# Kernel optimization log

Hardware: AMD Instinct MI355X
Metric: run time of the kernel (lower is better)

## Reference

```python
import jax, jax.numpy as jnp
import numpy as np
import math

B, S, DIN, DQ, DV = 8, 2048, 1024, 1024, 1024


def setup_inputs() -> dict:
    key = jax.random.key(0)
    ks = jax.random.split(key, 9)
    c_q = math.sqrt(6.0 / (DIN + DQ))
    c_v = math.sqrt(6.0 / (DIN + DV))
    query = jax.random.normal(ks[0], (B, S, DIN), dtype=jnp.float32)
    key_t = jax.random.normal(ks[1], (B, S, DIN), dtype=jnp.float32)
    value = jax.random.normal(ks[2], (B, S, DIN), dtype=jnp.float32)
    # Linear weights stored as [in, out] for x @ W; uniform init per module
    Wq = jax.random.uniform(ks[3], (DIN, DQ), jnp.float32, -c_q, c_q)
    Wk = jax.random.uniform(ks[4], (DIN, DQ), jnp.float32, -c_q, c_q)
    Wv = jax.random.uniform(ks[5], (DIN, DV), jnp.float32, -c_v, c_v)
    bq = jax.random.uniform(ks[6], (DQ,), jnp.float32, -c_q, c_q)
    bk = jax.random.uniform(ks[7], (DQ,), jnp.float32, -c_q, c_q)
    bv = jax.random.uniform(ks[8], (DV,), jnp.float32, -c_v, c_v)
    # causal mask: True where attention is disallowed (masked_fill semantics)
    mask = jnp.broadcast_to(jnp.triu(jnp.ones((S, S), dtype=bool), k=1), (B, S, S))
    return {"query": query, "key": key_t, "value": value,
            "Wq": Wq, "bq": bq, "Wk": Wk, "bk": bk, "Wv": Wv, "bv": bv,
            "mask": mask}


def reference(query, key, value, Wq, bq, Wk, bk, Wv, bv, mask):
    q = query @ Wq + bq                       # [B,S,DQ]
    k = key @ Wk + bk                         # [B,S,DQ]
    v = value @ Wv + bv                       # [B,S,DV]
    scores = jnp.einsum('bsd,btd->bst', q, k) / math.sqrt(DQ)  # [B,S,S]
    scores = jnp.where(mask, jnp.float32(-1e9), scores)
    weights = jax.nn.softmax(scores, axis=2)
    y = jnp.einsum('bst,btd->bsd', weights, v)  # [B,S,DV]
    return y
```

## Files before the change

kernel.cpp:

```cpp
#include <hip/hip_runtime.h>


typedef unsigned short u16;
typedef unsigned int   u32;
typedef float f32x4 __attribute__((ext_vector_type(4)));
typedef short s16x8 __attribute__((ext_vector_type(8)));

__device__ __forceinline__ u16 f2bf(float x) {
  u32 u = __builtin_bit_cast(u32, x);
  u += 0x7fffu + ((u >> 16) & 1u);
  return (u16)(u >> 16);
}

__device__ __forceinline__ void gld_lds16(const u16* g, u16* l) {
  __builtin_amdgcn_global_load_lds((const __attribute__((address_space(1))) void*)g,
                                   (__attribute__((address_space(3))) void*)l,
                                   16, 0, 0);
}

__global__ __launch_bounds__(256) void cvt_bf16_3(const float* __restrict__ i0,
                                                  const float* __restrict__ i1,
                                                  const float* __restrict__ i2,
                                                  u16* __restrict__ out, long X) {
  const float* in = blockIdx.y == 0 ? i0 : (blockIdx.y == 1 ? i1 : i2);
  long i = (long)blockIdx.x * 256 + threadIdx.x;
  float4 v = ((const float4*)in)[i];
  ushort4 o;
  o.x = f2bf(v.x); o.y = f2bf(v.y); o.z = f2bf(v.z); o.w = f2bf(v.w);
  ((ushort4*)(out + blockIdx.y * X))[i] = o;
}

__global__ __launch_bounds__(256) void transpose_w3(const float* __restrict__ w0,
                                                    const float* __restrict__ w1,
                                                    const float* __restrict__ w2,
                                                    u16* __restrict__ Wt,
                                                    int K, int N, long WN) {
  __shared__ u16 t[32][33];
  const float* W = blockIdx.z == 0 ? w0 : (blockIdx.z == 1 ? w1 : w2);
  u16* out = Wt + blockIdx.z * WN;
  int n0 = blockIdx.x * 32, k0 = blockIdx.y * 32;
  int tx = threadIdx.x & 31, ty = threadIdx.x >> 5;
  for (int r = ty; r < 32; r += 8)
    t[r][tx] = f2bf(W[(long)(k0 + r) * N + n0 + tx]);
  __syncthreads();
  for (int r = ty; r < 32; r += 8)
    out[(long)(n0 + r) * K + k0 + tx] = t[tx][r];
}

__global__ __launch_bounds__(256) void transpose_v(const u16* __restrict__ v,
                                                   u16* __restrict__ vt,
                                                   int S, int D) {
  __shared__ u16 t[32][33];
  long b = blockIdx.z;
  const u16* vb = v + b * S * D;
  u16* vtb = vt + b * S * D;
  int d0 = blockIdx.x * 32, s0 = blockIdx.y * 32;
  int tx = threadIdx.x & 31, ty = threadIdx.x >> 5;
  for (int r = ty; r < 32; r += 8)
    t[r][tx] = vb[(long)(s0 + r) * D + d0 + tx];
  __syncthreads();
  for (int r = ty; r < 32; r += 8)
    vtb[(long)(d0 + r) * S + s0 + tx] = t[tx][r];
}

__device__ __forceinline__ void gemm_core(const u16* __restrict__ At,
                                          const u16* __restrict__ Bt,
                                          int lda, int ldb, int ktEnd,
                                          f32x4 (&acc)[4][4],
                                          u16* lA, u16* lB) {
  const int tid = threadIdx.x;
  const int lane = tid & 63, half = lane >> 4, l16 = lane & 15;
  const int wave = tid >> 6;
  const int wm = (wave >> 1) * 64, wn = (wave & 1) * 64;

  const int c0 = tid, c1 = tid + 256;
  const int r0 = c0 >> 2, kp0 = (c0 & 3) ^ ((c0 >> 3) & 3);
  const int r1 = c1 >> 2, kp1 = (c1 & 3) ^ ((c1 >> 3) & 3);
  const u16* gA0 = At + (long)r0 * lda + kp0 * 8;
  const u16* gA1 = At + (long)r1 * lda + kp1 * 8;
  const u16* gB0 = Bt + (long)r0 * ldb + kp0 * 8;
  const u16* gB1 = Bt + (long)r1 * ldb + kp1 * 8;
  u16* lA0 = lA + c0 * 8; u16* lA1 = lA + c1 * 8;
  u16* lB0 = lB + c0 * 8; u16* lB1 = lB + c1 * 8;
  const int swz = (half ^ ((l16 >> 1) & 3)) * 8;

  for (int kt = 0; kt < ktEnd; ++kt) {
    const int k0 = kt * 32;
    gld_lds16(gA0 + k0, lA0);
    gld_lds16(gA1 + k0, lA1);
    gld_lds16(gB0 + k0, lB0);
    gld_lds16(gB1 + k0, lB1);
    __syncthreads();
    s16x8 af[4], bfr[4];
#pragma unroll
    for (int mi = 0; mi < 4; ++mi)
      af[mi] = *(const s16x8*)&lA[(wm + mi * 16 + l16) * 32 + swz];
#pragma unroll
    for (int ni = 0; ni < 4; ++ni)
      bfr[ni] = *(const s16x8*)&lB[(wn + ni * 16 + l16) * 32 + swz];
#pragma unroll
    for (int mi = 0; mi < 4; ++mi)
#pragma unroll
      for (int ni = 0; ni < 4; ++ni)
        acc[mi][ni] = __builtin_amdgcn_mfma_f32_16x16x32_bf16(af[mi], bfr[ni], acc[mi][ni], 0, 0, 0);
    __syncthreads();
  }
}

struct ProjPtrs {
  const u16* A[3];
  const u16* B[3];
  u16* C[3];
  const float* bias[3];
};

__global__ __launch_bounds__(256, 2)
void gemm_proj(ProjPtrs p, int lda, int ldb, int ldc, int kTiles) {
  const int bn = blockIdx.x, bm = blockIdx.y, bz = blockIdx.z;
  __shared__ u16 lA[128 * 32], lB[128 * 32];
  f32x4 acc[4][4];
#pragma unroll
  for (int i = 0; i < 4; ++i)
#pragma unroll
    for (int j = 0; j < 4; ++j) { f32x4 z = {0.f, 0.f, 0.f, 0.f}; acc[i][j] = z; }

  gemm_core(p.A[bz] + (long)bm * 128 * lda, p.B[bz] + (long)bn * 128 * ldb,
            lda, ldb, kTiles, acc, lA, lB);

  const int lane = threadIdx.x & 63, half = lane >> 4, l16 = lane & 15;
  const int wave = threadIdx.x >> 6;
  const int wm = (wave >> 1) * 64, wn = (wave & 1) * 64;
  const int colBase = bn * 128 + wn + l16;
  const int rowBase = bm * 128 + wm + half * 4;
  u16* Cb = p.C[bz];
  const float* bias = p.bias[bz];
#pragma unroll
  for (int mi = 0; mi < 4; ++mi)
#pragma unroll
    for (int ni = 0; ni < 4; ++ni) {
      int col = colBase + ni * 16;
      float bv = bias[col];
#pragma unroll
      for (int r = 0; r < 4; ++r)
        Cb[(long)(rowBase + mi * 16 + r) * ldc + col] = f2bf(acc[mi][ni][r] + bv);
    }
}

__global__ __launch_bounds__(256, 2)
void gemm_scores(const u16* __restrict__ q, const u16* __restrict__ k,
                 float* __restrict__ scores, int ld, long sQK, long sSC,
                 int kTiles, float scale) {
  const int t = blockIdx.x, bz = blockIdx.y;
  int bm = (int)((sqrtf(8.f * t + 1.f) - 1.f) * 0.5f);
  while ((bm + 1) * (bm + 2) / 2 <= t) ++bm;
  while (bm * (bm + 1) / 2 > t) --bm;
  const int bn = t - bm * (bm + 1) / 2;

  __shared__ u16 lA[128 * 32], lB[128 * 32];
  f32x4 acc[4][4];
#pragma unroll
  for (int i = 0; i < 4; ++i)
#pragma unroll
    for (int j = 0; j < 4; ++j) { f32x4 z = {0.f, 0.f, 0.f, 0.f}; acc[i][j] = z; }

  gemm_core(q + (long)bz * sQK + (long)bm * 128 * ld,
            k + (long)bz * sQK + (long)bn * 128 * ld,
            ld, ld, kTiles, acc, lA, lB);

  const int lane = threadIdx.x & 63, half = lane >> 4, l16 = lane & 15;
  const int wave = threadIdx.x >> 6;
  const int wm = (wave >> 1) * 64, wn = (wave & 1) * 64;
  float* Cb = scores + (long)bz * sSC;
  const int colBase = bn * 128 + wn + l16;
  const int rowBase = bm * 128 + wm + half * 4;
#pragma unroll
  for (int mi = 0; mi < 4; ++mi)
#pragma unroll
    for (int ni = 0; ni < 4; ++ni) {
      int col = colBase + ni * 16;
#pragma unroll
      for (int r = 0; r < 4; ++r)
        Cb[(long)(rowBase + mi * 16 + r) * 2048 + col] = acc[mi][ni][r] * scale;
    }
}

__global__ __launch_bounds__(256, 2)
void gemm_pv(const u16* __restrict__ P, const u16* __restrict__ vT,
             float* __restrict__ y, int lda, int ldb, int ldc,
             long sP, long sV, long sY, int kTiles) {
  const int bn = blockIdx.x, bz = blockIdx.z;
  const int bm = gridDim.y - 1 - blockIdx.y;
  int ktEnd = (bm + 1) * 4; if (ktEnd > kTiles) ktEnd = kTiles;

  __shared__ u16 lA[128 * 32], lB[128 * 32];
  f32x4 acc[4][4];
#pragma unroll
  for (int i = 0; i < 4; ++i)
#pragma unroll
    for (int j = 0; j < 4; ++j) { f32x4 z = {0.f, 0.f, 0.f, 0.f}; acc[i][j] = z; }

  gemm_core(P + (long)bz * sP + (long)bm * 128 * lda,
            vT + (long)bz * sV + (long)bn * 128 * ldb,
            lda, ldb, ktEnd, acc, lA, lB);

  const int lane = threadIdx.x & 63, half = lane >> 4, l16 = lane & 15;
  const int wave = threadIdx.x >> 6;
  const int wm = (wave >> 1) * 64, wn = (wave & 1) * 64;
  float* Cb = y + (long)bz * sY;
  const int colBase = bn * 128 + wn + l16;
  const int rowBase = bm * 128 + wm + half * 4;
#pragma unroll
  for (int mi = 0; mi < 4; ++mi)
#pragma unroll
    for (int ni = 0; ni < 4; ++ni) {
      int col = colBase + ni * 16;
#pragma unroll
      for (int r = 0; r < 4; ++r)
        Cb[(long)(rowBase + mi * 16 + r) * ldc + col] = acc[mi][ni][r];
    }
}

__global__ __launch_bounds__(256) void softmax_causal(const float* __restrict__ scores,
                                                      u16* __restrict__ P, int S) {
  __shared__ float buf[2048];
  __shared__ float red[4];
  const int tid = threadIdx.x;
  const long row = blockIdx.x;
  const int i = (int)(row & (S - 1));
  const int n = i + 1;
  const float* srow = scores + row * S;
  u16* prow = P + row * S;

  float m = -1e30f;
  for (int j = tid; j < n; j += 256) { float x = srow[j]; buf[j] = x; m = fmaxf(m, x); }
  for (int o = 32; o > 0; o >>= 1) m = fmaxf(m, __shfl_down(m, o));
  if ((tid & 63) == 0) red[tid >> 6] = m;
  __syncthreads();
  m = fmaxf(fmaxf(red[0], red[1]), fmaxf(red[2], red[3]));
  __syncthreads();
  float s = 0.f;
  for (int j = tid; j < n; j += 256) { float e = __expf(buf[j] - m); buf[j] = e; s += e; }
  for (int o = 32; o > 0; o >>= 1) s += __shfl_down(s, o);
  if ((tid & 63) == 0) red[tid >> 6] = s;
  __syncthreads();
  s = red[0] + red[1] + red[2] + red[3];
  float inv = 1.f / s;
  for (int j = tid; j < n; j += 256) prow[j] = f2bf(buf[j] * inv);
  const int zend = ((i >> 7) + 1) << 7;
  for (int j = n + tid; j < zend; j += 256) prow[j] = 0;
}

extern "C" void kernel_launch(void* const* d_in, const int* in_sizes, int n_in,
                              void* d_out, int out_size, void* d_ws, size_t ws_size,
                              hipStream_t stream) {
  const int B = 8, S = 2048, DIN = 1024, DQ = 1024, DV = 1024;
  const long X  = (long)B * S * DIN;
  const long WN = (long)DIN * DQ;

  const float* query = (const float*)d_in[0];
  const float* key   = (const float*)d_in[1];
  const float* value = (const float*)d_in[2];
  const float* Wq = (const float*)d_in[3];
  const float* bq = (const float*)d_in[4];
  const float* Wk = (const float*)d_in[5];
  const float* bk = (const float*)d_in[6];
  const float* Wv = (const float*)d_in[7];
  const float* bv = (const float*)d_in[8];

  u16* w = (u16*)d_ws;
  u16* xq = w;
  u16* WT = w + 3 * X;
  const long R1 = 3 * X + 3 * WN;
  u16* vbuf = w + R1;
  u16* q  = w + R1 + X;
  u16* k  = w + R1 + 2 * X;
  u16* vT = w + R1 + 3 * X;
  float* scores = (float*)d_ws;
  u16* P = q;

  dim3 blk(256);
  cvt_bf16_3<<<dim3(X / 1024, 3), blk, 0, stream>>>(query, key, value, xq, X);
  transpose_w3<<<dim3(DQ / 32, DIN / 32, 3), blk, 0, stream>>>(Wq, Wk, Wv, WT, DIN, DQ, WN);

  ProjPtrs pp;
  pp.A[0] = xq; pp.A[1] = xq + X; pp.A[2] = xq + 2 * X;
  pp.B[0] = WT; pp.B[1] = WT + WN; pp.B[2] = WT + 2 * WN;
  pp.C[0] = q;  pp.C[1] = k;      pp.C[2] = vbuf;
  pp.bias[0] = bq; pp.bias[1] = bk; pp.bias[2] = bv;
  gemm_proj<<<dim3(DQ / 128, (B * S) / 128, 3), blk, 0, stream>>>(
      pp, DIN, DIN, DQ, DIN / 32);

  transpose_v<<<dim3(DV / 32, S / 32, B), blk, 0, stream>>>(vbuf, vT, S, DV);

  gemm_scores<<<dim3(136, B), blk, 0, stream>>>(
      q, k, scores, DQ, X / B, (long)S * S, DQ / 32, 0.03125f);

  softmax_causal<<<dim3(B * S), blk, 0, stream>>>(scores, P, S);

  gemm_pv<<<dim3(DV / 128, S / 128, B), blk, 0, stream>>>(
      P, vT, (float*)d_out, S, S, DV, (long)S * S, (long)DV * S, (long)S * DV,
      S / 32);
}
```

Before: 681.8 us.

## Loop four N-tiles per projection block and vectorize register-resident causal softmax

```diff
diff --git a/kernel.cpp b/kernel.cpp
--- a/kernel.cpp
+++ b/kernel.cpp
@@ -116,34 +116,39 @@
 
 __global__ __launch_bounds__(256, 2)
 void gemm_proj(ProjPtrs p, int lda, int ldb, int ldc, int kTiles) {
-  const int bn = blockIdx.x, bm = blockIdx.y, bz = blockIdx.z;
+  const int bx = blockIdx.x, bm = blockIdx.y, bz = blockIdx.z;
   __shared__ u16 lA[128 * 32], lB[128 * 32];
-  f32x4 acc[4][4];
-#pragma unroll
-  for (int i = 0; i < 4; ++i)
-#pragma unroll
-    for (int j = 0; j < 4; ++j) { f32x4 z = {0.f, 0.f, 0.f, 0.f}; acc[i][j] = z; }
-
-  gemm_core(p.A[bz] + (long)bm * 128 * lda, p.B[bz] + (long)bn * 128 * ldb,
-            lda, ldb, kTiles, acc, lA, lB);
+  const u16* At = p.A[bz] + (long)bm * 128 * lda;
+  u16* Cb = p.C[bz];
+  const float* bias = p.bias[bz];
 
   const int lane = threadIdx.x & 63, half = lane >> 4, l16 = lane & 15;
   const int wave = threadIdx.x >> 6;
   const int wm = (wave >> 1) * 64, wn = (wave & 1) * 64;
-  const int colBase = bn * 128 + wn + l16;
   const int rowBase = bm * 128 + wm + half * 4;
-  u16* Cb = p.C[bz];
-  const float* bias = p.bias[bz];
-#pragma unroll
-  for (int mi = 0; mi < 4; ++mi)
-#pragma unroll
-    for (int ni = 0; ni < 4; ++ni) {
-      int col = colBase + ni * 16;
-      float bv = bias[col];
-#pragma unroll
-      for (int r = 0; r < 4; ++r)
-        Cb[(long)(rowBase + mi * 16 + r) * ldc + col] = f2bf(acc[mi][ni][r] + bv);
-    }
+
+  for (int nt = 0; nt < 4; ++nt) {
+    const int bn = bx * 4 + nt;
+    f32x4 acc[4][4];
+#pragma unroll
+    for (int i = 0; i < 4; ++i)
+#pragma unroll
+      for (int j = 0; j < 4; ++j) { f32x4 z = {0.f, 0.f, 0.f, 0.f}; acc[i][j] = z; }
+
+    gemm_core(At, p.B[bz] + (long)bn * 128 * ldb, lda, ldb, kTiles, acc, lA, lB);
+
+    const int colBase = bn * 128 + wn + l16;
+#pragma unroll
+    for (int mi = 0; mi < 4; ++mi)
+#pragma unroll
+      for (int ni = 0; ni < 4; ++ni) {
+        int col = colBase + ni * 16;
+        float bv = bias[col];
+#pragma unroll
+        for (int r = 0; r < 4; ++r)
+          Cb[(long)(rowBase + mi * 16 + r) * ldc + col] = f2bf(acc[mi][ni][r] + bv);
+      }
+  }
 }
 
 __global__ __launch_bounds__(256, 2)
@@ -222,32 +227,67 @@
 
 __global__ __launch_bounds__(256) void softmax_causal(const float* __restrict__ scores,
                                                       u16* __restrict__ P, int S) {
-  __shared__ float buf[2048];
   __shared__ float red[4];
   const int tid = threadIdx.x;
   const long row = blockIdx.x;
   const int i = (int)(row & (S - 1));
-  const int n = i + 1;
-  const float* srow = scores + row * S;
-  u16* prow = P + row * S;
-
+  const int zend = ((i >> 7) + 1) << 7;
+  const int n4 = zend >> 2;
+  const float4* srow = (const float4*)(scores + row * S);
+
+  float4 v[2];
   float m = -1e30f;
-  for (int j = tid; j < n; j += 256) { float x = srow[j]; buf[j] = x; m = fmaxf(m, x); }
+#pragma unroll
+  for (int s = 0; s < 2; ++s) {
+    const int j4 = tid + s * 256;
+    float4 x;
+    if (j4 < n4) {
+      x = srow[j4];
+      const int j = j4 * 4;
+      if (j + 3 > i) {
+        x.x = (j     <= i) ? x.x : -1e30f;
+        x.y = (j + 1 <= i) ? x.y : -1e30f;
+        x.z = (j + 2 <= i) ? x.z : -1e30f;
+        x.w = (j + 3 <= i) ? x.w : -1e30f;
+      }
+    } else {
+      x.x = x.y = x.z = x.w = -1e30f;
+    }
+    v[s] = x;
+    m = fmaxf(m, fmaxf(fmaxf(x.x, x.y), fmaxf(x.z, x.w)));
+  }
   for (int o = 32; o > 0; o >>= 1) m = fmaxf(m, __shfl_down(m, o));
   if ((tid & 63) == 0) red[tid >> 6] = m;
   __syncthreads();
   m = fmaxf(fmaxf(red[0], red[1]), fmaxf(red[2], red[3]));
   __syncthreads();
-  float s = 0.f;
-  for (int j = tid; j < n; j += 256) { float e = __expf(buf[j] - m); buf[j] = e; s += e; }
-  for (int o = 32; o > 0; o >>= 1) s += __shfl_down(s, o);
-  if ((tid & 63) == 0) red[tid >> 6] = s;
-  __syncthreads();
-  s = red[0] + red[1] + red[2] + red[3];
-  float inv = 1.f / s;
-  for (int j = tid; j < n; j += 256) prow[j] = f2bf(buf[j] * inv);
-  const int zend = ((i >> 7) + 1) << 7;
-  for (int j = n + tid; j < zend; j += 256) prow[j] = 0;
+
+  float sum = 0.f;
+#pragma unroll
+  for (int s = 0; s < 2; ++s) {
+    float4 e;
+    e.x = __expf(v[s].x - m); e.y = __expf(v[s].y - m);
+    e.z = __expf(v[s].z - m); e.w = __expf(v[s].w - m);
+    sum += (e.x + e.y) + (e.z + e.w);
+    v[s] = e;
+  }
+  for (int o = 32; o > 0; o >>= 1) sum += __shfl_down(sum, o);
+  if ((tid & 63) == 0) red[tid >> 6] = sum;
+  __syncthreads();
+  sum = red[0] + red[1] + red[2] + red[3];
+  const float inv = 1.f / sum;
+
+  ushort4* prow = (ushort4*)(P + row * S);
+#pragma unroll
+  for (int s = 0; s < 2; ++s) {
+    const int j4 = tid + s * 256;
+    if (j4 < n4) {
+      ushort4 o;
+      o.x = f2bf(v[s].x * inv); o.y = f2bf(v[s].y * inv);
+      o.z = f2bf(v[s].z * inv); o.w = f2bf(v[s].w * inv);
+      prow[j4] = o;
+    }
+  }
 }
 
 extern "C" void kernel_launch(void* const* d_in, const int* in_sizes, int n_in,
@@ -287,7 +327,7 @@
   pp.B[0] = WT; pp.B[1] = WT + WN; pp.B[2] = WT + 2 * WN;
   pp.C[0] = q;  pp.C[1] = k;      pp.C[2] = vbuf;
   pp.bias[0] = bq; pp.bias[1] = bk; pp.bias[2] = bv;
-  gemm_proj<<<dim3(DQ / 128, (B * S) / 128, 3), blk, 0, stream>>>(
+  gemm_proj<<<dim3(DQ / 512, (B * S) / 128, 3), blk, 0, stream>>>(
       pp, DIN, DIN, DQ, DIN / 32);
 
   transpose_v<<<dim3(DV / 32, S / 32, B), blk, 0, stream>>>(vbuf, vT, S, DV);
```

New measurement: 681.9 us. About the same (+0.0%).

## Fuse exp into scores GEMM, defer softmax normalization, remap grids for XCD locality

Applied to the files above, without the earlier changes.

```diff
diff --git a/kernel.cpp b/kernel.cpp
--- a/kernel.cpp
+++ b/kernel.cpp
@@ -10,6 +10,10 @@
   u32 u = __builtin_bit_cast(u32, x);
   u += 0x7fffu + ((u >> 16) & 1u);
   return (u16)(u >> 16);
+}
+__device__ __forceinline__ float bf2f(u16 h) {
+  u32 u = (u32)h << 16;
+  return __builtin_bit_cast(float, u);
 }
 
 __device__ __forceinline__ void gld_lds16(const u16* g, u16* l) {
@@ -116,7 +120,14 @@
 
 __global__ __launch_bounds__(256, 2)
 void gemm_proj(ProjPtrs p, int lda, int ldb, int ldc, int kTiles) {
-  const int bn = blockIdx.x, bm = blockIdx.y, bz = blockIdx.z;
+  const int f = blockIdx.x;
+  const int xcd = f & 7;
+  const int g = f >> 3;
+  const int bz = g >> 7;
+  const int l = g & 127;
+  const int bm = (xcd << 4) + (l >> 3);
+  const int bn = l & 7;
+
   __shared__ u16 lA[128 * 32], lB[128 * 32];
   f32x4 acc[4][4];
 #pragma unroll
@@ -147,10 +158,12 @@
 }
 
 __global__ __launch_bounds__(256, 2)
-void gemm_scores(const u16* __restrict__ q, const u16* __restrict__ k,
-                 float* __restrict__ scores, int ld, long sQK, long sSC,
-                 int kTiles, float scale) {
-  const int t = blockIdx.x, bz = blockIdx.y;
+void gemm_scores_exp(const u16* __restrict__ q, const u16* __restrict__ k,
+                     u16* __restrict__ E, int ld, long sQK, long sSC,
+                     int kTiles, float scale) {
+  const int f = blockIdx.x;
+  const int bz = f & 7;
+  const int t = f >> 3;
   int bm = (int)((sqrtf(8.f * t + 1.f) - 1.f) * 0.5f);
   while ((bm + 1) * (bm + 2) / 2 <= t) ++bm;
   while (bm * (bm + 1) / 2 > t) --bm;
@@ -170,27 +183,51 @@
   const int lane = threadIdx.x & 63, half = lane >> 4, l16 = lane & 15;
   const int wave = threadIdx.x >> 6;
   const int wm = (wave >> 1) * 64, wn = (wave & 1) * 64;
-  float* Cb = scores + (long)bz * sSC;
+  u16* Eb = E + (long)bz * sSC;
   const int colBase = bn * 128 + wn + l16;
   const int rowBase = bm * 128 + wm + half * 4;
+  const bool diag = (bn == bm);
 #pragma unroll
   for (int mi = 0; mi < 4; ++mi)
 #pragma unroll
     for (int ni = 0; ni < 4; ++ni) {
       int col = colBase + ni * 16;
 #pragma unroll
-      for (int r = 0; r < 4; ++r)
-        Cb[(long)(rowBase + mi * 16 + r) * 2048 + col] = acc[mi][ni][r] * scale;
+      for (int r = 0; r < 4; ++r) {
+        int row = rowBase + mi * 16 + r;
+        float e = __expf(acc[mi][ni][r] * scale);
+        u16 out = (!diag || col <= row) ? f2bf(e) : (u16)0;
+        Eb[(long)row * 2048 + col] = out;
+      }
     }
 }
 
+__global__ __launch_bounds__(256) void row_inv(const u16* __restrict__ E,
+                                               float* __restrict__ inv, int S) {
+  const int wave = threadIdx.x >> 6, lane = threadIdx.x & 63;
+  const long row = (long)blockIdx.x * 4 + wave;
+  const int i = (int)(row & (S - 1));
+  const int zend = ((i >> 7) + 1) << 7;
+  const u16* erow = E + row * S;
+  float s = 0.f;
+  for (int c = lane * 4; c < zend; c += 256) {
+    ushort4 u = *(const ushort4*)(erow + c);
+    s += (bf2f(u.x) + bf2f(u.y)) + (bf2f(u.z) + bf2f(u.w));
+  }
+  for (int o = 32; o > 0; o >>= 1) s += __shfl_down(s, o);
+  if (lane == 0) inv[row] = 1.f / s;
+}
+
 __global__ __launch_bounds__(256, 2)
-void gemm_pv(const u16* __restrict__ P, const u16* __restrict__ vT,
-             float* __restrict__ y, int lda, int ldb, int ldc,
-             long sP, long sV, long sY, int kTiles) {
-  const int bn = blockIdx.x, bz = blockIdx.z;
-  const int bm = gridDim.y - 1 - blockIdx.y;
-  int ktEnd = (bm + 1) * 4; if (ktEnd > kTiles) ktEnd = kTiles;
+void gemm_pv(const u16* __restrict__ E, const u16* __restrict__ vT,
+             const float* __restrict__ inv, float* __restrict__ y,
+             int lda, int ldb, int ldc, long sP, long sV, long sY, int S) {
+  const int f = blockIdx.x;
+  const int bz = f & 7;
+  const int g = f >> 3;
+  const int bm = 15 - (g >> 3);
+  const int bn = g & 7;
+  const int ktEnd = (bm + 1) * 4;
 
   __shared__ u16 lA[128 * 32], lB[128 * 32];
   f32x4 acc[4][4];
@@ -199,7 +236,7 @@
 #pragma unroll
     for (int j = 0; j < 4; ++j) { f32x4 z = {0.f, 0.f, 0.f, 0.f}; acc[i][j] = z; }
 
-  gemm_core(P + (long)bz * sP + (long)bm * 128 * lda,
+  gemm_core(E + (long)bz * sP + (long)bm * 128 * lda,
             vT + (long)bz * sV + (long)bn * 128 * ldb,
             lda, ldb, ktEnd, acc, lA, lB);
 
@@ -207,47 +244,22 @@
   const int wave = threadIdx.x >> 6;
   const int wm = (wave >> 1) * 64, wn = (wave & 1) * 64;
   float* Cb = y + (long)bz * sY;
+  const float* invb = inv + (long)bz * S;
   const int colBase = bn * 128 + wn + l16;
   const int rowBase = bm * 128 + wm + half * 4;
 #pragma unroll
-  for (int mi = 0; mi < 4; ++mi)
+  for (int mi = 0; mi < 4; ++mi) {
+    float iv[4];
+#pragma unroll
+    for (int r = 0; r < 4; ++r) iv[r] = invb[rowBase + mi * 16 + r];
 #pragma unroll
     for (int ni = 0; ni < 4; ++ni) {
       int col = colBase + ni * 16;
 #pragma unroll
       for (int r = 0; r < 4; ++r)
-        Cb[(long)(rowBase + mi * 16 + r) * ldc + col] = acc[mi][ni][r];
+        Cb[(long)(rowBase + mi * 16 + r) * ldc + col] = acc[mi][ni][r] * iv[r];
     }
-}
-
-__global__ __launch_bounds__(256) void softmax_causal(const float* __restrict__ scores,
-                                                      u16* __restrict__ P, int S) {
-  __shared__ float buf[2048];
-  __shared__ float red[4];
-  const int tid = threadIdx.x;
-  const long row = blockIdx.x;
-  const int i = (int)(row & (S - 1));
-  const int n = i + 1;
-  const float* srow = scores + row * S;
-  u16* prow = P + row * S;
-
-  float m = -1e30f;
-  for (int j = tid; j < n; j += 256) { float x = srow[j]; buf[j] = x; m = fmaxf(m, x); }
-  for (int o = 32; o > 0; o >>= 1) m = fmaxf(m, __shfl_down(m, o));
-  if ((tid & 63) == 0) red[tid >> 6] = m;
-  __syncthreads();
-  m = fmaxf(fmaxf(red[0], red[1]), fmaxf(red[2], red[3]));
-  __syncthreads();
-  float s = 0.f;
-  for (int j = tid; j < n; j += 256) { float e = __expf(buf[j] - m); buf[j] = e; s += e; }
-  for (int o = 32; o > 0; o >>= 1) s += __shfl_down(s, o);
-  if ((tid & 63) == 0) red[tid >> 6] = s;
-  __syncthreads();
-  s = red[0] + red[1] + red[2] + red[3];
-  float inv = 1.f / s;
-  for (int j = tid; j < n; j += 256) prow[j] = f2bf(buf[j] * inv);
-  const int zend = ((i >> 7) + 1) << 7;
-  for (int j = n + tid; j < zend; j += 256) prow[j] = 0;
+  }
 }
 
 extern "C" void kernel_launch(void* const* d_in, const int* in_sizes, int n_in,
@@ -275,8 +287,8 @@
   u16* q  = w + R1 + X;
   u16* k  = w + R1 + 2 * X;
   u16* vT = w + R1 + 3 * X;
-  float* scores = (float*)d_ws;
-  u16* P = q;
+  u16* E = w;
+  float* inv = (float*)(w + 3 * X);
 
   dim3 blk(256);
   cvt_bf16_3<<<dim3(X / 1024, 3), blk, 0, stream>>>(query, key, value, xq, X);
@@ -287,17 +299,16 @@
   pp.B[0] = WT; pp.B[1] = WT + WN; pp.B[2] = WT + 2 * WN;
   pp.C[0] = q;  pp.C[1] = k;      pp.C[2] = vbuf;
   pp.bias[0] = bq; pp.bias[1] = bk; pp.bias[2] = bv;
-  gemm_proj<<<dim3(DQ / 128, (B * S) / 128, 3), blk, 0, stream>>>(
-      pp, DIN, DIN, DQ, DIN / 32);
+  gemm_proj<<<dim3(3072), blk, 0, stream>>>(pp, DIN, DIN, DQ, DIN / 32);
 
   transpose_v<<<dim3(DV / 32, S / 32, B), blk, 0, stream>>>(vbuf, vT, S, DV);
 
-  gemm_scores<<<dim3(136, B), blk, 0, stream>>>(
-      q, k, scores, DQ, X / B, (long)S * S, DQ / 32, 0.03125f);
-
-  softmax_causal<<<dim3(B * S), blk, 0, stream>>>(scores, P, S);
-
-  gemm_pv<<<dim3(DV / 128, S / 128, B), blk, 0, stream>>>(
-      P, vT, (float*)d_out, S, S, DV, (long)S * S, (long)DV * S, (long)S * DV,
-      S / 32);
-}
+  gemm_scores_exp<<<dim3(136 * 8), blk, 0, stream>>>(
+      q, k, E, DQ, X / B, (long)S * S, DQ / 32, 0.03125f);
+
+  row_inv<<<dim3(B * S / 4), blk, 0, stream>>>(E, inv, S);
+
+  gemm_pv<<<dim3(1024), blk, 0, stream>>>(
+      E, vT, inv, (float*)d_out, S, S, DV, (long)S * S, (long)DV * S,
+      (long)S * DV, S);
+}
```

Result: faster. 591.1 us (-13.3%).
